# Performance work log

Measured on AMD Instinct MI355X. Metric: run time of the kernel, lower is better.

The kernel has to match this reference:

```python
import jax, jax.numpy as jnp
from jax import lax
import numpy as np

B, D, NFM = 4096, 64, 32
N_USER, N_ITEM = 1000000, 100000
DN = ('NCHW', 'OIHW', 'NCHW')


def setup_inputs() -> dict:
    key = jax.random.key(0)
    ks = jax.random.split(key, 10)
    user = jax.random.randint(ks[0], (B, 1), 0, N_USER)
    item_pos = jax.random.randint(ks[1], (B, 1), 0, N_ITEM)
    item_neg = jax.random.randint(ks[2], (B, 1), 0, N_ITEM)
    user_emb_w = jax.random.normal(ks[3], (N_USER, D), dtype=jnp.float32) * 0.1
    item_emb_w = jax.random.normal(ks[4], (N_ITEM, D), dtype=jnp.float32) * 0.1
    # conv1: in_channels=1; convs 2..6: in_channels=NFM (kaiming-ish init)
    conv1_w = jax.random.normal(ks[5], (NFM, 1, 4, 4), dtype=jnp.float32) * 0.35
    conv1_b = jnp.full((NFM,), 0.01, dtype=jnp.float32)
    rest_w = jax.random.normal(ks[6], (5, NFM, NFM, 4, 4), dtype=jnp.float32) * 0.0625
    rest_b = jnp.full((5, NFM), 0.01, dtype=jnp.float32)
    pred_w = jax.random.normal(ks[7], (1, NFM), dtype=jnp.float32) * 0.25
    pred_b = jnp.full((1,), 0.01, dtype=jnp.float32)
    return dict(user=user, item_pos=item_pos, item_neg=item_neg,
                user_emb_w=user_emb_w, item_emb_w=item_emb_w,
                conv1_w=conv1_w, conv1_b=conv1_b, rest_w=rest_w, rest_b=rest_b,
                pred_w=pred_w, pred_b=pred_b)


def _conv(x, w, b):
    y = lax.conv_general_dilated(x, w, window_strides=(2, 2),
                                 padding=[(1, 1), (1, 1)], dimension_numbers=DN)
    return jax.nn.relu(y + b[None, :, None, None])


def _branch(u, it, conv1_w, conv1_b, rest_w, rest_b, pred_w, pred_b):
    # batched outer product replaces the per-sample torch.mm loop: [B,1,64,64]
    x = jnp.einsum('bd,be->bde', u, it)[:, None, :, :]
    x = _conv(x, conv1_w, conv1_b)
    for i in range(rest_w.shape[0]):  # fixed 5 conv layers
        x = _conv(x, rest_w[i], rest_b[i])
    x = x.reshape(x.shape[0], -1)  # [B, NFM] (spatial collapsed to 1x1)
    return jax.nn.sigmoid(x @ pred_w.T + pred_b)


def reference(user, item_pos, item_neg, user_emb_w, item_emb_w,
              conv1_w, conv1_b, rest_w, rest_b, pred_w, pred_b):
    u = user_emb_w[user[:, 0]]          # [B, 64]
    ip = item_emb_w[item_pos[:, 0]]     # [B, 64]
    ineg = item_emb_w[item_neg[:, 0]]   # [B, 64]
    out1 = _branch(u, ip, conv1_w, conv1_b, rest_w, rest_b, pred_w, pred_b)
    out2 = _branch(u, ineg, conv1_w, conv1_b, rest_w, rest_b, pred_w, pred_b)
    return (out1, out2)
```

## Files before the change

### kernel.cpp

```cpp
#include <hip/hip_runtime.h>
#include <math.h>

#define NT 256
#define NW 4

typedef __attribute__((ext_vector_type(8))) short short8;
typedef __attribute__((ext_vector_type(4))) float f32x4;

#define U_OFF    0
#define IT_OFF   256
#define B1_OFF   512
#define RB_OFF   640
#define PW_OFF   1280
#define PBI_OFF  1408
#define ZP_OFF   1424
#define X1_OFF   1536
#define X1_STR   2064
#define X2_OFF   36624
#define X2_STR   1040
#define X3_OFF   X1_OFF
#define X3_STR   528
#define X4_OFF   (X1_OFF + 4224)
#define X4_STR   272
#define X5_OFF   (X1_OFF + 5312)
#define X5_STR   144
#define X6_OFF   (X1_OFF + 5600)
#define SMEM_BYTES 53264

__device__ __forceinline__ unsigned short f2bf(float f) {
    unsigned int x = __float_as_uint(f);
    x += 0x7fffu + ((x >> 16) & 1u);
    return (unsigned short)(x >> 16);
}

__device__ __forceinline__ void loadB16(short8 bfr[16], const unsigned short* __restrict__ wsbf,
                                        const float* __restrict__ rwg, int useWs,
                                        int L, int co, int g) {
    if (useWs) {
        const unsigned short* base = wsbf + L * 16384 + co * 32 + g * 8;
#pragma unroll
        for (int tap = 0; tap < 16; ++tap)
            bfr[tap] = *(const short8*)(base + tap * 1024);
    } else {
#pragma unroll
        for (int tap = 0; tap < 16; ++tap) {
            union { short8 s; unsigned short u[8]; } cv;
#pragma unroll
            for (int e = 0; e < 8; ++e)
                cv.u[e] = f2bf(rwg[((L * 32 + co) * 32 + g * 8 + e) * 16 + tap]);
            bfr[tap] = cv.s;
        }
    }
}

template<int PH, int QW, int NIN, int INS, int OUTS, bool LAST>
__device__ __forceinline__ void convL(char* smb, int inOff, int outOff,
                                      const short8 bfr[16], float bias,
                                      int p0, int shift) {
    const int t = threadIdx.x;
    const int w = t >> 6, l = t & 63;
    const int n = l & 15, g = l >> 4, nt = w & 1;
    constexpr int M = PH * QW;
    constexpr int MT = (M + 15) / 16;
    for (int tile = w; tile < 2 * MT; tile += NW) {
        const int mt = tile >> 1;
        f32x4 acc = {bias, bias, bias, bias};
        const int m = mt * 16 + (l & 15);
        const int mm = (m < M) ? m : 0;
        const int p = mm % PH, q = mm / PH;
#pragma unroll
        for (int a = 0; a < 4; ++a)
#pragma unroll
            for (int dj = 0; dj < 4; ++dj) {
                const int row = 2 * (p0 + p) + a - 1;
                const int col = 2 * q + dj - 1;
                const bool ok = (m < M) && ((unsigned)row < (unsigned)NIN)
                                        && ((unsigned)col < (unsigned)NIN);
                const int rb = row - shift;
                unsigned addr = (unsigned)(inOff + rb * INS + col * 64 + g * 16);
                addr ^= (unsigned)(((rb >> 3) & 1) << 4);
                addr = ok ? addr : (unsigned)(ZP_OFF + g * 16);
                short8 af = *(const short8*)(smb + addr);
                acc = __builtin_amdgcn_mfma_f32_16x16x32_bf16(af, bfr[a * 4 + dj], acc, 0, 0, 0);
            }
#pragma unroll
        for (int vi = 0; vi < 4; ++vi) {
            const int mo = mt * 16 + g * 4 + vi;
            if (mo < M) {
                const float v = fmaxf(acc[vi], 0.f);
                if constexpr (LAST) {
                    *(float*)(smb + outOff + (nt * 16 + n) * 4) = v;
                } else {
                    const int po = mo % PH + p0, qo = mo / PH;
                    unsigned addr = (unsigned)(outOff + po * OUTS + qo * 64 + (nt * 16 + n) * 2);
                    addr ^= (unsigned)(((po >> 3) & 1) << 4);
                    *(unsigned short*)(smb + addr) = f2bf(v);
                }
            }
        }
    }
}

__global__ void preconv_w(const float* __restrict__ rwg, unsigned short* __restrict__ wsbf) {
    int idx = blockIdx.x * 256 + threadIdx.x;
    if (idx < 81920) {
        int ci = idx & 31, co = (idx >> 5) & 31, tap = (idx >> 10) & 15, L = idx >> 14;
        wsbf[idx] = f2bf(rwg[(((L * 32 + co) * 32 + ci) << 4) + tap]);
    }
}

__global__ void __launch_bounds__(NT, 3)
convncf_main(const int* __restrict__ user, const int* __restrict__ item_pos,
             const int* __restrict__ item_neg,
             const float* __restrict__ uemb, const float* __restrict__ iemb,
             const float* __restrict__ w1g, const float* __restrict__ b1g,
             const float* __restrict__ rwg, const float* __restrict__ rbg,
             const float* __restrict__ pwg, const float* __restrict__ pbg,
             const unsigned short* __restrict__ wsbf, int useWs,
             float* __restrict__ out, int B)
{
    extern __shared__ char smb[];
    float* smf = (float*)smb;
    const int t = threadIdx.x, w = t >> 6, l = t & 63;
    const int co = ((t >> 6) & 1) * 16 + (t & 15);
    const int g = l >> 4;
    const int s = blockIdx.x, branch = blockIdx.y;
    const int uidx = user[s];
    const int iidx = branch ? item_neg[s] : item_pos[s];

    short8 bfr[16];

    for (int i = t; i < 353; i += NT) {
        if (i < 64)       smf[U_OFF/4 + i]        = uemb[(long)uidx * 64 + i];
        else if (i < 128) smf[IT_OFF/4 + i - 64]  = iemb[(long)iidx * 64 + i - 64];
        else if (i < 160) smf[B1_OFF/4 + i - 128] = b1g[i - 128];
        else if (i < 320) smf[RB_OFF/4 + i - 160] = rbg[i - 160];
        else if (i < 352) smf[PW_OFF/4 + i - 320] = pwg[i - 320];
        else              smf[PBI_OFF/4] = pbg[0];
    }
    if (t < 4) *(float4*)(smb + ZP_OFF + t * 16) = make_float4(0.f, 0.f, 0.f, 0.f);
    __syncthreads();

    {
        const int pi = t & 127;
        const int cgp = pi & 3, jp = pi >> 2;
        const int rlh = t >> 7;
        const int rl0 = rlh ? 9 : 0;
        const int rl1 = rlh ? 17 : 9;

        float tval[4][8];
        {
            float itv[4];
#pragma unroll
            for (int dj = 0; dj < 4; ++dj) {
                const int c = 2 * jp - 1 + dj;
                itv[dj] = (c >= 0 && c < 64) ? smf[IT_OFF/4 + c] : 0.f;
            }
#pragma unroll
            for (int e = 0; e < 8; ++e) {
                const float* wp = w1g + (cgp * 8 + e) * 16;
#pragma unroll
                for (int a = 0; a < 4; ++a) {
                    const float4 wv = *(const float4*)(wp + a * 4);
                    float v = wv.x * itv[0];
                    v = fmaf(wv.y, itv[1], v);
                    v = fmaf(wv.z, itv[2], v);
                    v = fmaf(wv.w, itv[3], v);
                    tval[a][e] = v;
                }
            }
        }

        {
            float bb[8];
            {
                const float* b1p = smf + B1_OFF/4 + cgp * 8;
#pragma unroll
                for (int e = 0; e < 8; ++e) bb[e] = b1p[e];
            }
            for (int rl = rl0; rl < rl1; ++rl) {
                float acc[8];
#pragma unroll
                for (int e = 0; e < 8; ++e) acc[e] = bb[e];
#pragma unroll
                for (int a = 0; a < 4; ++a) {
                    const int m = 2 * rl - 1 + a;
                    const float uv = (m >= 0) ? smf[U_OFF/4 + m] : 0.f;
#pragma unroll
                    for (int e = 0; e < 8; ++e)
                        acc[e] = fmaf(uv, tval[a][e], acc[e]);
                }
                union { short8 sv; unsigned short u[8]; } cv;
#pragma unroll
                for (int e = 0; e < 8; ++e) cv.u[e] = f2bf(fmaxf(acc[e], 0.f));
                unsigned addr = (unsigned)(X1_OFF + rl * X1_STR + jp * 64 + cgp * 16);
                addr ^= (unsigned)(((rl >> 3) & 1) << 4);
                *(short8*)(smb + addr) = cv.sv;
            }
        }
        loadB16(bfr, wsbf, rwg, useWs, 0, co, g);
        __syncthreads();

        convL<8, 16, 32, X1_STR, X2_STR, false>(smb, X1_OFF, X2_OFF, bfr,
                                                smf[RB_OFF/4 + co], 0, 0);
        __syncthreads();

        {
            float bb[8];
            {
                const float* b1p = smf + B1_OFF/4 + cgp * 8;
#pragma unroll
                for (int e = 0; e < 8; ++e) bb[e] = b1p[e];
            }
            for (int rl = rl0; rl < rl1; ++rl) {
                const int r = rl + 15;
                float acc[8];
#pragma unroll
                for (int e = 0; e < 8; ++e) acc[e] = bb[e];
#pragma unroll
                for (int a = 0; a < 4; ++a) {
                    const int m = 2 * r - 1 + a;
                    const float uv = (m < 64) ? smf[U_OFF/4 + m] : 0.f;
#pragma unroll
                    for (int e = 0; e < 8; ++e)
                        acc[e] = fmaf(uv, tval[a][e], acc[e]);
                }
                union { short8 sv; unsigned short u[8]; } cv;
#pragma unroll
                for (int e = 0; e < 8; ++e) cv.u[e] = f2bf(fmaxf(acc[e], 0.f));
                unsigned addr = (unsigned)(X1_OFF + rl * X1_STR + jp * 64 + cgp * 16);
                addr ^= (unsigned)(((rl >> 3) & 1) << 4);
                *(short8*)(smb + addr) = cv.sv;
            }
        }
        __syncthreads();

        convL<8, 16, 32, X1_STR, X2_STR, false>(smb, X1_OFF, X2_OFF, bfr,
                                                smf[RB_OFF/4 + co], 8, 15);
        loadB16(bfr, wsbf, rwg, useWs, 1, co, g);
        __syncthreads();
    }

    convL<8, 8, 16, X2_STR, X3_STR, false>(smb, X2_OFF, X3_OFF, bfr, smf[RB_OFF/4 + 32 + co], 0, 0);
    loadB16(bfr, wsbf, rwg, useWs, 2, co, g);
    __syncthreads();

    convL<4, 4, 8, X3_STR, X4_STR, false>(smb, X3_OFF, X4_OFF, bfr, smf[RB_OFF/4 + 64 + co], 0, 0);
    loadB16(bfr, wsbf, rwg, useWs, 3, co, g);
    __syncthreads();

    convL<2, 2, 4, X4_STR, X5_STR, false>(smb, X4_OFF, X5_OFF, bfr, smf[RB_OFF/4 + 96 + co], 0, 0);
    loadB16(bfr, wsbf, rwg, useWs, 4, co, g);
    __syncthreads();

    convL<1, 1, 2, X5_STR, 0, true>(smb, X5_OFF, X6_OFF, bfr, smf[RB_OFF/4 + 128 + co], 0, 0);
    __syncthreads();

    if (w == 0) {
        float v = (l < 32) ? smf[X6_OFF/4 + l] * smf[PW_OFF/4 + l] : 0.f;
#pragma unroll
        for (int d = 32; d >= 1; d >>= 1) v += __shfl_xor(v, d, 64);
        if (l == 0) {
            const float z = smf[PBI_OFF/4] + v;
            out[branch * B + s] = 1.f / (1.f + expf(-z));
        }
    }
}

extern "C" void kernel_launch(void* const* d_in, const int* in_sizes, int n_in,
                              void* d_out, int out_size, void* d_ws, size_t ws_size,
                              hipStream_t stream) {
    const int*   user     = (const int*)d_in[0];
    const int*   item_pos = (const int*)d_in[1];
    const int*   item_neg = (const int*)d_in[2];
    const float* uemb     = (const float*)d_in[3];
    const float* iemb     = (const float*)d_in[4];
    const float* w1       = (const float*)d_in[5];
    const float* b1       = (const float*)d_in[6];
    const float* rw       = (const float*)d_in[7];
    const float* rb       = (const float*)d_in[8];
    const float* pw       = (const float*)d_in[9];
    const float* pb       = (const float*)d_in[10];
    float* out = (float*)d_out;
    const int B = in_sizes[0];

    const int useWs = (ws_size >= 81920u * sizeof(unsigned short)) ? 1 : 0;
    unsigned short* wsbf = (unsigned short*)d_ws;
    if (useWs)
        preconv_w<<<dim3(320), dim3(256), 0, stream>>>(rw, wsbf);

    (void)hipFuncSetAttribute((const void*)convncf_main,
                              hipFuncAttributeMaxDynamicSharedMemorySize, SMEM_BYTES);
    dim3 grid(B, 2);
    convncf_main<<<grid, NT, SMEM_BYTES, stream>>>(
        user, item_pos, item_neg, uemb, iemb, w1, b1, rw, rb, pw, pb,
        wsbf, useWs, out, B);
}
```

Measured before the change: 301.2 us.

## Use 32x32x16 bf16 MFMA for the second conv layer

Adds a conv routine built on the 32x32x16 bf16 MFMA, where each wave covers a 32-output-pixel by 32-channel tile. It replaces the 16x16-based convL for layer 2 in both half passes. B operands now come straight from global pre-converted weights (or are converted on the fly) on every tap, not from preloaded registers. The aim is fewer MFMA issues and better operand reuse, at the cost of repeated global weight loads inside the inner loop and a different wave-to-tile split.

```diff
diff --git a/kernel.cpp b/kernel.cpp
--- a/kernel.cpp
+++ b/kernel.cpp
@@ -6,6 +6,7 @@
 
 typedef __attribute__((ext_vector_type(8))) short short8;
 typedef __attribute__((ext_vector_type(4))) float f32x4;
+typedef __attribute__((ext_vector_type(16))) float f32x16;
 
 #define U_OFF    0
 #define IT_OFF   256
@@ -101,6 +102,69 @@
     }
 }
 
+template<int PH, int QW, int NIN, int INS, int OUTS>
+__device__ __forceinline__ void conv32s(char* smb, int inOff, int outOff,
+                                        const unsigned short* __restrict__ wsbf,
+                                        const float* __restrict__ rwg, int useWs,
+                                        int L, int p0, int shift) {
+    const float* smf = (const float*)smb;
+    const int t = threadIdx.x;
+    const int w = t >> 6, l = t & 63;
+    const int kg = l >> 5, colo = l & 31;
+    const float bias = smf[RB_OFF / 4 + L * 32 + colo];
+    constexpr int M = PH * QW;
+    constexpr int TILES = (M + 31) / 32;
+    for (int tile = w; tile < TILES; tile += NW) {
+        f32x16 acc;
+#pragma unroll
+        for (int r = 0; r < 16; ++r) acc[r] = bias;
+        const int m = tile * 32 + (l & 31);
+        const int mm = (m < M) ? m : 0;
+        const int p = mm % PH, q = mm / PH;
+#pragma unroll
+        for (int a = 0; a < 4; ++a)
+#pragma unroll
+            for (int dj = 0; dj < 4; ++dj) {
+                const int row = 2 * (p0 + p) + a - 1;
+                const int col = 2 * q + dj - 1;
+                const bool ok = (m < M) && ((unsigned)row < (unsigned)NIN)
+                                        && ((unsigned)col < (unsigned)NIN);
+                const int rb = row - shift;
+                const int tap = a * 4 + dj;
+#pragma unroll
+                for (int kh = 0; kh < 2; ++kh) {
+                    unsigned addr = (unsigned)(inOff + rb * INS + col * 64 + kh * 32 + kg * 16);
+                    addr ^= (unsigned)(((rb >> 3) & 1) << 4);
+                    addr = ok ? addr : (unsigned)(ZP_OFF + kh * 32 + kg * 16);
+                    short8 af = *(const short8*)(smb + addr);
+                    short8 bf;
+                    if (useWs) {
+                        bf = *(const short8*)(wsbf + ((L * 16 + tap) * 32 + colo) * 32
+                                              + kh * 16 + kg * 8);
+                    } else {
+                        union { short8 s; unsigned short u[8]; } cv;
+#pragma unroll
+                        for (int e = 0; e < 8; ++e)
+                            cv.u[e] = f2bf(rwg[((L * 32 + colo) * 32 + kh * 16 + kg * 8 + e) * 16 + tap]);
+                        bf = cv.s;
+                    }
+                    acc = __builtin_amdgcn_mfma_f32_32x32x16_bf16(af, bf, acc, 0, 0, 0);
+                }
+            }
+#pragma unroll
+        for (int r = 0; r < 16; ++r) {
+            const int mo = tile * 32 + (r & 3) + 8 * (r >> 2) + 4 * kg;
+            if (mo < M) {
+                const float v = fmaxf(acc[r], 0.f);
+                const int po = mo % PH + p0, qo = mo / PH;
+                unsigned addr = (unsigned)(outOff + po * OUTS + qo * 64 + colo * 2);
+                addr ^= (unsigned)(((po >> 3) & 1) << 4);
+                *(unsigned short*)(smb + addr) = f2bf(v);
+            }
+        }
+    }
+}
+
 __global__ void preconv_w(const float* __restrict__ rwg, unsigned short* __restrict__ wsbf) {
     int idx = blockIdx.x * 256 + threadIdx.x;
     if (idx < 81920) {
@@ -198,11 +262,9 @@
                 *(short8*)(smb + addr) = cv.sv;
             }
         }
-        loadB16(bfr, wsbf, rwg, useWs, 0, co, g);
         __syncthreads();
 
-        convL<8, 16, 32, X1_STR, X2_STR, false>(smb, X1_OFF, X2_OFF, bfr,
-                                                smf[RB_OFF/4 + co], 0, 0);
+        conv32s<8, 16, 32, X1_STR, X2_STR>(smb, X1_OFF, X2_OFF, wsbf, rwg, useWs, 0, 0, 0);
         __syncthreads();
 
         {
@@ -235,8 +297,7 @@
         }
         __syncthreads();
 
-        convL<8, 16, 32, X1_STR, X2_STR, false>(smb, X1_OFF, X2_OFF, bfr,
-                                                smf[RB_OFF/4 + co], 8, 15);
+        conv32s<8, 16, 32, X1_STR, X2_STR>(smb, X1_OFF, X2_OFF, wsbf, rwg, useWs, 0, 8, 15);
         loadB16(bfr, wsbf, rwg, useWs, 1, co, g);
         __syncthreads();
     }
```

After: 388.3 us. 1.29x slower.
